# Optimization experiments

Measured on AMD Instinct MI355X. Metric: run time of the kernel, lower is better.

## Reference

```python
import jax, jax.numpy as jnp
import numpy as np

ALPHA1 = 0.1
ALPHA2 = 0.1
NOISE = 0.02
B, T, H, O = 128, 512, 512, 3


def setup_inputs() -> dict:
    key = jax.random.key(0)
    ks = jax.random.split(key, 10)
    return {
        "x": jax.random.normal(ks[0], (B, T, 5), dtype=jnp.float32),
        "wi_stim": jax.random.normal(ks[1], (3, H), dtype=jnp.float32) / np.sqrt(3),
        "wrec11": jax.random.normal(ks[2], (H, H), dtype=jnp.float32) / np.sqrt(H),
        "wi_ctx": jax.random.normal(ks[3], (2, H), dtype=jnp.float32) / np.sqrt(2),
        "wrec22": jax.random.normal(ks[4], (H, H), dtype=jnp.float32) / np.sqrt(H),
        "wrec12": jax.random.normal(ks[5], (H, H), dtype=jnp.float32) / np.sqrt(H),
        "wrec21": jax.random.normal(ks[6], (H, H), dtype=jnp.float32) / np.sqrt(H),
        "wo": jax.random.normal(ks[7], (H, O), dtype=jnp.float32) / np.sqrt(H),
        "noise1": jax.random.normal(ks[8], (T, B, H), dtype=jnp.float32),
        "noise2": jax.random.normal(ks[9], (T, B, H), dtype=jnp.float32),
    }


def reference(x, wi_stim, wrec11, wi_ctx, wrec22, wrec12, wrec21, wo, noise1, noise2):
    # x: [B, T, 5]; noise: [T, B, H] (pre-sampled standard normals, scaled by NOISE)
    xs = jnp.transpose(x[:, :, :3], (1, 0, 2))  # [T, B, 3]
    xc = jnp.transpose(x[:, :, 3:], (1, 0, 2))  # [T, B, 2]

    def step(carry, inp):
        h1, h2 = carry
        xsi, xci, n1, n2 = inp
        h1 = (1 - ALPHA1) * h1 + ALPHA1 * (
            xsi @ wi_stim + jnp.tanh(h1) @ wrec11 + jnp.tanh(h2) @ wrec12 + n1 * NOISE
        )
        # note: h2 update uses the freshly-updated h1 (as in the torch loop)
        h2 = (1 - ALPHA2) * h2 + ALPHA2 * (
            xci @ wi_ctx + jnp.tanh(h1) @ wrec21 + jnp.tanh(h2) @ wrec22 + n2 * NOISE
        )
        return (h1, h2), jnp.tanh(h2) @ wo

    h0 = jnp.zeros((x.shape[0], wrec11.shape[0]), dtype=x.dtype)
    _, out_t = jax.lax.scan(step, (h0, h0), (xs, xc, noise1, noise2))  # [T, B, O]
    return jnp.transpose(out_t, (1, 0, 2))  # [B, T, O]
```

## Files before the change

### kernel.cpp

```cpp
#include <hip/hip_runtime.h>
#include <hip/hip_bf16.h>

#define TT 512
#define BB 128
#define HH 512
#define NGROUP 8
#define NSLICE 8
#define ALPHA 0.1f
#define NOISE_S 0.02f

typedef __attribute__((ext_vector_type(8))) short short8;
typedef __attribute__((ext_vector_type(8))) _Float16 half8;
typedef __attribute__((ext_vector_type(4))) float f32x4;

#define WPACK_CH 132096
#define PUB1_B (WPACK_CH * 16)
#define PUB2_B (PUB1_B + NGROUP * 32768)

__device__ __forceinline__ unsigned short f2h(float f) {
  return __builtin_bit_cast(unsigned short, (_Float16)f);
}

__device__ __forceinline__ float fast_tanh(float x) {
  float e = __builtin_amdgcn_exp2f(x * 2.8853900817779268f);
  return 1.0f - 2.0f * __builtin_amdgcn_rcpf(e + 1.0f);
}

__device__ __forceinline__ f32x4 mfma16(short8 a, short8 b, f32x4 c) {
  return __builtin_amdgcn_mfma_f32_16x16x32_f16(
      __builtin_bit_cast(half8, a), __builtin_bit_cast(half8, b), c, 0, 0, 0);
}

__global__ void pack_weights(const float* __restrict__ w11, const float* __restrict__ w12,
                             const float* __restrict__ w21, const float* __restrict__ w22,
                             const float* __restrict__ wo, unsigned short* __restrict__ dst) {
  int idx = blockIdx.x * 256 + threadIdx.x;
  if (idx < 131072) {
    int which = idx >> 16;
    int c0 = idx & 65535;
    int kt = c0 >> 11, rem = c0 & 2047;
    int nt = rem >> 6, lane = rem & 63;
    const float* wlo = which ? w21 : w11;
    const float* whi = which ? w22 : w12;
    unsigned short* p = dst + (size_t)idx * 8;
    int n = nt * 16 + (lane & 15);
    int kb = kt * 32 + ((lane >> 4) & 3) * 8;
#pragma unroll
    for (int i = 0; i < 8; ++i) {
      int k = kb + i;
      float v = (k < HH) ? wlo[k * HH + n] : whi[(k - HH) * HH + n];
      p[i] = f2h(v);
    }
  } else if (idx < 132096) {
    int c0 = idx - 131072;
    int kt = c0 >> 6, lane = c0 & 63;
    unsigned short* p = dst + (size_t)131072 * 8 + (size_t)c0 * 8;
    int n = lane & 15;
    int kb = kt * 32 + ((lane >> 4) & 3) * 8;
#pragma unroll
    for (int i = 0; i < 8; ++i) {
      float v = (n < 3) ? wo[(kb + i) * 3 + n] : 0.0f;
      p[i] = f2h(v);
    }
  }
}

__global__ void zero_ws(int* __restrict__ p, int n) {
  for (int i = blockIdx.x * 256 + threadIdx.x; i < n; i += gridDim.x * 256)
    p[i] = 0;
}

__global__ __launch_bounds__(256, 1)
void rnn_main(const float* __restrict__ x, const float* __restrict__ wi_stim,
              const float* __restrict__ wi_ctx, const float* __restrict__ noise1,
              const float* __restrict__ noise2, char* __restrict__ ws,
              float* __restrict__ out) {
  __shared__ __align__(16) unsigned short T1buf[16 * 512];
  __shared__ __align__(16) unsigned short T2buf[16 * 512];
  __shared__ __align__(16) unsigned short WOlds[16 * 512];
  __shared__ float xstage[2][16][5];

  const int tid = threadIdx.x;
  const int w = tid >> 6, lane = tid & 63;
  const int c16 = lane & 15, kh = lane >> 4;
  const int g = blockIdx.x & (NGROUP - 1);
  const int slice = blockIdx.x >> 3;
  const int nt = slice * 4 + w;
  const int n0 = nt * 16;
  const int b0 = g * 16;
  const int lrow0 = kh * 4;

  const short8* __restrict__ WC = (const short8*)ws;
  unsigned* __restrict__ pub1 = (unsigned*)(ws + PUB1_B) + g * 8192;
  unsigned* __restrict__ pub2 = (unsigned*)(ws + PUB2_B) + g * 8192;

  short8 z = {0, 0, 0, 0, 0, 0, 0, 0};
  for (int i = tid; i < 1024; i += 256) {
    ((short8*)T1buf)[i] = z;
    ((short8*)T2buf)[i] = z;
  }
#pragma unroll
  for (int c = 0; c < 4; ++c) {
    int kt = w * 4 + c;
    short8 v = WC[131072 + kt * 64 + lane];
    *(short8*)&WOlds[kt * 512 + lane * 8] = v;
  }
  if (tid < 80) {
    int b = tid / 5, c = tid % 5;
    xstage[0][b][c] = x[((size_t)(b0 + b) * TT + 0) * 5 + c];
  }

  short8 wA[32], wB[32];
#pragma unroll
  for (int kt = 0; kt < 32; ++kt) {
    wA[kt] = WC[kt * 2048 + nt * 64 + lane];
    wB[kt] = WC[65536 + kt * 2048 + nt * 64 + lane];
  }
#pragma unroll
  for (int kt = 0; kt < 32; ++kt) {
    asm volatile("" : "+v"(wA[kt]));
    asm volatile("" : "+v"(wB[kt]));
  }

  float wis[3], wic[2];
#pragma unroll
  for (int c = 0; c < 3; ++c) wis[c] = wi_stim[c * HH + n0 + c16];
#pragma unroll
  for (int c = 0; c < 2; ++c) wic[c] = wi_ctx[c * HH + n0 + c16];

  float h1[4] = {0, 0, 0, 0}, h2[4] = {0, 0, 0, 0};

  const int kt_p = nt >> 1;
  const int hi = (((nt & 1) * 16) + c16) >> 3;
  const int ci = c16 & 7;

  auto stage_poll = [&](const unsigned* pubw, unsigned short* Tbuf, unsigned exp) {
    unsigned long long v[4][4];
    bool ok;
    do {
      ok = true;
#pragma unroll
      for (int c = 0; c < 4; ++c) {
        const unsigned long long* src =
            (const unsigned long long*)(pubw + ((w * 4 + c) << 9)) + lane * 4;
#pragma unroll
        for (int j = 0; j < 4; ++j) {
          v[c][j] = __hip_atomic_load(&src[j], __ATOMIC_RELAXED,
                                      __HIP_MEMORY_SCOPE_AGENT);
          ok &= (((unsigned)(v[c][j] >> 16) & 0xffffu) >= exp);
          ok &= ((unsigned)(v[c][j] >> 48) >= exp);
        }
      }
    } while (!ok);
    __builtin_amdgcn_sched_barrier(0);
    asm volatile("" ::: "memory");
#pragma unroll
    for (int c = 0; c < 4; ++c) {
      unsigned long long u0 = (v[c][0] & 0xffffull)
                            | (((v[c][0] >> 32) & 0xffffull) << 16)
                            | ((v[c][1] & 0xffffull) << 32)
                            | (((v[c][1] >> 32) & 0xffffull) << 48);
      unsigned long long u1 = (v[c][2] & 0xffffull)
                            | (((v[c][2] >> 32) & 0xffffull) << 16)
                            | ((v[c][3] & 0xffffull) << 32)
                            | (((v[c][3] >> 32) & 0xffffull) << 48);
      *(unsigned long long*)&Tbuf[(w * 4 + c) * 512 + lane * 8] = u0;
      *(unsigned long long*)&Tbuf[(w * 4 + c) * 512 + lane * 8 + 4] = u1;
    }
  };

  __syncthreads();

  for (int t = 0; t < TT; ++t) {
    const int buf = t & 1;
    const unsigned tagA = (unsigned)(t + 1) << 16;

    float n1v[4];
#pragma unroll
    for (int r = 0; r < 4; ++r)
      n1v[r] = noise1[((size_t)t * BB + b0 + lrow0 + r) * HH + n0 + c16];

    f32x4 aA = {0, 0, 0, 0}, aB = {0, 0, 0, 0};
#pragma unroll
    for (int kt = 0; kt < 16; ++kt) {
      short8 a1 = *(const short8*)&T1buf[kt * 512 + lane * 8];
      aA = mfma16(a1, wA[kt], aA);
    }
    stage_poll(pub2, T2buf, (unsigned)t);
    __syncthreads();
#pragma unroll
    for (int kt = 0; kt < 16; ++kt) {
      short8 a2 = *(const short8*)&T2buf[kt * 512 + lane * 8];
      aB = mfma16(a2, wA[16 + kt], aB);
    }

    if (t > 0 && slice == ((t - 1) & 7) && w == 0) {
      f32x4 ao = {0, 0, 0, 0};
#pragma unroll
      for (int kt = 0; kt < 16; ++kt) {
        short8 a2 = *(const short8*)&T2buf[kt * 512 + lane * 8];
        short8 bo = *(const short8*)&WOlds[kt * 512 + lane * 8];
        ao = mfma16(a2, bo, ao);
      }
      if (c16 < 3) {
#pragma unroll
        for (int r = 0; r < 4; ++r)
          out[((size_t)(b0 + lrow0 + r) * TT + (t - 1)) * 3 + c16] = ao[r];
      }
    }

    unsigned short tp[4];
#pragma unroll
    for (int r = 0; r < 4; ++r) {
      float pre = aA[r] + aB[r]
                + wis[0] * xstage[buf][lrow0 + r][0]
                + wis[1] * xstage[buf][lrow0 + r][1]
                + wis[2] * xstage[buf][lrow0 + r][2]
                + NOISE_S * n1v[r];
      float h = (1.0f - ALPHA) * h1[r] + ALPHA * pre;
      h1[r] = h;
      tp[r] = f2h(fast_tanh(h));
    }
#pragma unroll
    for (int r = 0; r < 4; ++r)
      __hip_atomic_store(&pub1[kt_p * 512 + (lrow0 + r + hi * 16) * 8 + ci],
                         tagA | tp[r], __ATOMIC_RELAXED, __HIP_MEMORY_SCOPE_AGENT);

    float n2v[4];
#pragma unroll
    for (int r = 0; r < 4; ++r)
      n2v[r] = noise2[((size_t)t * BB + b0 + lrow0 + r) * HH + n0 + c16];

    f32x4 bA = {0, 0, 0, 0}, bB = {0, 0, 0, 0};
#pragma unroll
    for (int kt = 0; kt < 16; ++kt) {
      short8 a2 = *(const short8*)&T2buf[kt * 512 + lane * 8];
      bB = mfma16(a2, wB[16 + kt], bB);
    }
    stage_poll(pub1, T1buf, (unsigned)(t + 1));
    if (t + 1 < TT && tid < 80) {
      int b = tid / 5, c = tid % 5;
      xstage[buf ^ 1][b][c] = x[((size_t)(b0 + b) * TT + (t + 1)) * 5 + c];
    }
    __syncthreads();
#pragma unroll
    for (int kt = 0; kt < 16; ++kt) {
      short8 a1 = *(const short8*)&T1buf[kt * 512 + lane * 8];
      bA = mfma16(a1, wB[kt], bA);
    }
#pragma unroll
    for (int r = 0; r < 4; ++r) {
      float pre = bA[r] + bB[r]
                + wic[0] * xstage[buf][lrow0 + r][3]
                + wic[1] * xstage[buf][lrow0 + r][4]
                + NOISE_S * n2v[r];
      float h = (1.0f - ALPHA) * h2[r] + ALPHA * pre;
      h2[r] = h;
      tp[r] = f2h(fast_tanh(h));
    }
#pragma unroll
    for (int r = 0; r < 4; ++r)
      __hip_atomic_store(&pub2[kt_p * 512 + (lrow0 + r + hi * 16) * 8 + ci],
                         tagA | tp[r], __ATOMIC_RELAXED, __HIP_MEMORY_SCOPE_AGENT);
  }

  if (slice == ((TT - 1) & 7)) {
    stage_poll(pub2, T2buf, (unsigned)TT);
    __syncthreads();
    if (w == 0) {
      f32x4 ao = {0, 0, 0, 0};
#pragma unroll
      for (int kt = 0; kt < 16; ++kt) {
        short8 a2 = *(const short8*)&T2buf[kt * 512 + lane * 8];
        short8 bo = *(const short8*)&WOlds[kt * 512 + lane * 8];
        ao = mfma16(a2, bo, ao);
      }
      if (c16 < 3) {
#pragma unroll
        for (int r = 0; r < 4; ++r)
          out[((size_t)(b0 + lrow0 + r) * TT + (TT - 1)) * 3 + c16] = ao[r];
      }
    }
  }
}

extern "C" void kernel_launch(void* const* d_in, const int* in_sizes, int n_in,
                              void* d_out, int out_size, void* d_ws, size_t ws_size,
                              hipStream_t stream) {
  const float* x       = (const float*)d_in[0];
  const float* wi_stim = (const float*)d_in[1];
  const float* w11     = (const float*)d_in[2];
  const float* wi_ctx  = (const float*)d_in[3];
  const float* w22     = (const float*)d_in[4];
  const float* w12     = (const float*)d_in[5];
  const float* w21     = (const float*)d_in[6];
  const float* wo      = (const float*)d_in[7];
  const float* n1      = (const float*)d_in[8];
  const float* n2      = (const float*)d_in[9];
  char* ws = (char*)d_ws;

  int nz = (NGROUP * 32768 * 2) / 4;
  zero_ws<<<64, 256, 0, stream>>>((int*)(ws + PUB1_B), nz);
  pack_weights<<<516, 256, 0, stream>>>(w11, w12, w21, w22, wo,
                                        (unsigned short*)ws);
  rnn_main<<<NSLICE * NGROUP, 256, 0, stream>>>(x, wi_stim, wi_ctx, n1, n2, ws,
                                                (float*)d_out);
}
```

Before: 3.578 ms.

## Process two batch groups per block to interleave independent recurrences

Each block now handles two independent 16-row batch groups instead of one, which halves the grid to 32 blocks. Per step, the block alternates between the two groups' h1 and h2 phases, so one group's cross-block poll latency can be hidden behind the other group's MFMA work. The cost is twice the serial MFMA and tanh work per block, more syncthreads per step, and fewer CUs in use.

```diff
diff --git a/kernel.cpp b/kernel.cpp
--- a/kernel.cpp
+++ b/kernel.cpp
@@ -6,6 +6,7 @@
 #define HH 512
 #define NGROUP 8
 #define NSLICE 8
+#define GPB 2
 #define ALPHA 0.1f
 #define NOISE_S 0.02f
 
@@ -75,27 +76,29 @@
               const float* __restrict__ wi_ctx, const float* __restrict__ noise1,
               const float* __restrict__ noise2, char* __restrict__ ws,
               float* __restrict__ out) {
-  __shared__ __align__(16) unsigned short T1buf[16 * 512];
-  __shared__ __align__(16) unsigned short T2buf[16 * 512];
+  __shared__ __align__(16) unsigned short T1buf[2][16 * 512];
+  __shared__ __align__(16) unsigned short T2buf[2][16 * 512];
   __shared__ __align__(16) unsigned short WOlds[16 * 512];
-  __shared__ float xstage[2][16][5];
+  __shared__ float xstage[2][2][16][5];
 
   const int tid = threadIdx.x;
   const int w = tid >> 6, lane = tid & 63;
   const int c16 = lane & 15, kh = lane >> 4;
-  const int g = blockIdx.x & (NGROUP - 1);
-  const int slice = blockIdx.x >> 3;
+  const int slice = blockIdx.x >> 2;
+  const int gp = blockIdx.x & 3;
   const int nt = slice * 4 + w;
   const int n0 = nt * 16;
-  const int b0 = g * 16;
   const int lrow0 = kh * 4;
 
   const short8* __restrict__ WC = (const short8*)ws;
-  unsigned* __restrict__ pub1 = (unsigned*)(ws + PUB1_B) + g * 8192;
-  unsigned* __restrict__ pub2 = (unsigned*)(ws + PUB2_B) + g * 8192;
+  unsigned* const pub1g[2] = {(unsigned*)(ws + PUB1_B) + gp * 8192,
+                              (unsigned*)(ws + PUB1_B) + (gp + 4) * 8192};
+  unsigned* const pub2g[2] = {(unsigned*)(ws + PUB2_B) + gp * 8192,
+                              (unsigned*)(ws + PUB2_B) + (gp + 4) * 8192};
+  const int b0g[2] = {gp * 16, (gp + 4) * 16};
 
   short8 z = {0, 0, 0, 0, 0, 0, 0, 0};
-  for (int i = tid; i < 1024; i += 256) {
+  for (int i = tid; i < 2048; i += 256) {
     ((short8*)T1buf)[i] = z;
     ((short8*)T2buf)[i] = z;
   }
@@ -105,9 +108,10 @@
     short8 v = WC[131072 + kt * 64 + lane];
     *(short8*)&WOlds[kt * 512 + lane * 8] = v;
   }
-  if (tid < 80) {
-    int b = tid / 5, c = tid % 5;
-    xstage[0][b][c] = x[((size_t)(b0 + b) * TT + 0) * 5 + c];
+  if (tid < 160) {
+    int gi = tid / 80, rem = tid % 80;
+    int b = rem / 5, c = rem % 5;
+    xstage[0][gi][b][c] = x[((size_t)(b0g[gi] + b) * TT + 0) * 5 + c];
   }
 
   short8 wA[32], wB[32];
@@ -128,11 +132,13 @@
 #pragma unroll
   for (int c = 0; c < 2; ++c) wic[c] = wi_ctx[c * HH + n0 + c16];
 
-  float h1[4] = {0, 0, 0, 0}, h2[4] = {0, 0, 0, 0};
+  float h1[2][4] = {{0, 0, 0, 0}, {0, 0, 0, 0}};
+  float h2[2][4] = {{0, 0, 0, 0}, {0, 0, 0, 0}};
 
   const int kt_p = nt >> 1;
   const int hi = (((nt & 1) * 16) + c16) >> 3;
   const int ci = c16 & 7;
+  const int pslot = kt_p * 512 + (lrow0 + hi * 16) * 8 + ci;
 
   auto stage_poll = [&](const unsigned* pubw, unsigned short* Tbuf, unsigned exp) {
     unsigned long long v[4][4];
@@ -173,112 +179,125 @@
 
   for (int t = 0; t < TT; ++t) {
     const int buf = t & 1;
-    const unsigned tagA = (unsigned)(t + 1) << 16;
-
-    float n1v[4];
-#pragma unroll
-    for (int r = 0; r < 4; ++r)
-      n1v[r] = noise1[((size_t)t * BB + b0 + lrow0 + r) * HH + n0 + c16];
-
-    f32x4 aA = {0, 0, 0, 0}, aB = {0, 0, 0, 0};
-#pragma unroll
-    for (int kt = 0; kt < 16; ++kt) {
-      short8 a1 = *(const short8*)&T1buf[kt * 512 + lane * 8];
-      aA = mfma16(a1, wA[kt], aA);
-    }
-    stage_poll(pub2, T2buf, (unsigned)t);
+    const unsigned tagN = (unsigned)(t + 1) << 16;
+
+#pragma unroll
+    for (int gi = 0; gi < 2; ++gi) {
+      float n1v[4];
+#pragma unroll
+      for (int r = 0; r < 4; ++r)
+        n1v[r] = noise1[((size_t)t * BB + b0g[gi] + lrow0 + r) * HH + n0 + c16];
+
+      f32x4 aA = {0, 0, 0, 0}, aB = {0, 0, 0, 0};
+#pragma unroll
+      for (int kt = 0; kt < 16; ++kt) {
+        short8 a1 = *(const short8*)&T1buf[gi][kt * 512 + lane * 8];
+        aA = mfma16(a1, wA[kt], aA);
+      }
+      stage_poll(pub2g[gi], T2buf[gi], (unsigned)t);
+      __syncthreads();
+#pragma unroll
+      for (int kt = 0; kt < 16; ++kt) {
+        short8 a2 = *(const short8*)&T2buf[gi][kt * 512 + lane * 8];
+        aB = mfma16(a2, wA[16 + kt], aB);
+      }
+
+      if (t > 0 && slice == ((t - 1) & 7) && w == gi) {
+        f32x4 ao = {0, 0, 0, 0};
+#pragma unroll
+        for (int kt = 0; kt < 16; ++kt) {
+          short8 a2 = *(const short8*)&T2buf[gi][kt * 512 + lane * 8];
+          short8 bo = *(const short8*)&WOlds[kt * 512 + lane * 8];
+          ao = mfma16(a2, bo, ao);
+        }
+        if (c16 < 3) {
+#pragma unroll
+          for (int r = 0; r < 4; ++r)
+            out[((size_t)(b0g[gi] + lrow0 + r) * TT + (t - 1)) * 3 + c16] = ao[r];
+        }
+      }
+
+      unsigned short tp[4];
+#pragma unroll
+      for (int r = 0; r < 4; ++r) {
+        float pre = aA[r] + aB[r]
+                  + wis[0] * xstage[buf][gi][lrow0 + r][0]
+                  + wis[1] * xstage[buf][gi][lrow0 + r][1]
+                  + wis[2] * xstage[buf][gi][lrow0 + r][2]
+                  + NOISE_S * n1v[r];
+        float h = (1.0f - ALPHA) * h1[gi][r] + ALPHA * pre;
+        h1[gi][r] = h;
+        tp[r] = f2h(fast_tanh(h));
+      }
+#pragma unroll
+      for (int r = 0; r < 4; ++r)
+        __hip_atomic_store(&pub1g[gi][pslot + r * 8], tagN | tp[r],
+                           __ATOMIC_RELAXED, __HIP_MEMORY_SCOPE_AGENT);
+    }
+
+#pragma unroll
+    for (int gi = 0; gi < 2; ++gi) {
+      float n2v[4];
+#pragma unroll
+      for (int r = 0; r < 4; ++r)
+        n2v[r] = noise2[((size_t)t * BB + b0g[gi] + lrow0 + r) * HH + n0 + c16];
+
+      f32x4 bA = {0, 0, 0, 0}, bB = {0, 0, 0, 0};
+#pragma unroll
+      for (int kt = 0; kt < 16; ++kt) {
+        short8 a2 = *(const short8*)&T2buf[gi][kt * 512 + lane * 8];
+        bB = mfma16(a2, wB[16 + kt], bB);
+      }
+      stage_poll(pub1g[gi], T1buf[gi], (unsigned)(t + 1));
+      if (gi == 1 && t + 1 < TT && tid < 160) {
+        int gj = tid / 80, rem = tid % 80;
+        int b = rem / 5, c = rem % 5;
+        xstage[buf ^ 1][gj][b][c] = x[((size_t)(b0g[gj] + b) * TT + (t + 1)) * 5 + c];
+      }
+      __syncthreads();
+#pragma unroll
+      for (int kt = 0; kt < 16; ++kt) {
+        short8 a1 = *(const short8*)&T1buf[gi][kt * 512 + lane * 8];
+        bA = mfma16(a1, wB[kt], bA);
+      }
+      unsigned short tp[4];
+#pragma unroll
+      for (int r = 0; r < 4; ++r) {
+        float pre = bA[r] + bB[r]
+                  + wic[0] * xstage[buf][gi][lrow0 + r][3]
+                  + wic[1] * xstage[buf][gi][lrow0 + r][4]
+                  + NOISE_S * n2v[r];
+        float h = (1.0f - ALPHA) * h2[gi][r] + ALPHA * pre;
+        h2[gi][r] = h;
+        tp[r] = f2h(fast_tanh(h));
+      }
+#pragma unroll
+      for (int r = 0; r < 4; ++r)
+        __hip_atomic_store(&pub2g[gi][pslot + r * 8], tagN | tp[r],
+                           __ATOMIC_RELAXED, __HIP_MEMORY_SCOPE_AGENT);
+    }
+  }
+
+  if (slice == ((TT - 1) & 7)) {
+#pragma unroll
+    for (int gi = 0; gi < 2; ++gi)
+      stage_poll(pub2g[gi], T2buf[gi], (unsigned)TT);
     __syncthreads();
 #pragma unroll
-    for (int kt = 0; kt < 16; ++kt) {
-      short8 a2 = *(const short8*)&T2buf[kt * 512 + lane * 8];
-      aB = mfma16(a2, wA[16 + kt], aB);
-    }
-
-    if (t > 0 && slice == ((t - 1) & 7) && w == 0) {
-      f32x4 ao = {0, 0, 0, 0};
-#pragma unroll
-      for (int kt = 0; kt < 16; ++kt) {
-        short8 a2 = *(const short8*)&T2buf[kt * 512 + lane * 8];
-        short8 bo = *(const short8*)&WOlds[kt * 512 + lane * 8];
-        ao = mfma16(a2, bo, ao);
-      }
-      if (c16 < 3) {
-#pragma unroll
-        for (int r = 0; r < 4; ++r)
-          out[((size_t)(b0 + lrow0 + r) * TT + (t - 1)) * 3 + c16] = ao[r];
-      }
-    }
-
-    unsigned short tp[4];
-#pragma unroll
-    for (int r = 0; r < 4; ++r) {
-      float pre = aA[r] + aB[r]
-                + wis[0] * xstage[buf][lrow0 + r][0]
-                + wis[1] * xstage[buf][lrow0 + r][1]
-                + wis[2] * xstage[buf][lrow0 + r][2]
-                + NOISE_S * n1v[r];
-      float h = (1.0f - ALPHA) * h1[r] + ALPHA * pre;
-      h1[r] = h;
-      tp[r] = f2h(fast_tanh(h));
-    }
-#pragma unroll
-    for (int r = 0; r < 4; ++r)
-      __hip_atomic_store(&pub1[kt_p * 512 + (lrow0 + r + hi * 16) * 8 + ci],
-                         tagA | tp[r], __ATOMIC_RELAXED, __HIP_MEMORY_SCOPE_AGENT);
-
-    float n2v[4];
-#pragma unroll
-    for (int r = 0; r < 4; ++r)
-      n2v[r] = noise2[((size_t)t * BB + b0 + lrow0 + r) * HH + n0 + c16];
-
-    f32x4 bA = {0, 0, 0, 0}, bB = {0, 0, 0, 0};
-#pragma unroll
-    for (int kt = 0; kt < 16; ++kt) {
-      short8 a2 = *(const short8*)&T2buf[kt * 512 + lane * 8];
-      bB = mfma16(a2, wB[16 + kt], bB);
-    }
-    stage_poll(pub1, T1buf, (unsigned)(t + 1));
-    if (t + 1 < TT && tid < 80) {
-      int b = tid / 5, c = tid % 5;
-      xstage[buf ^ 1][b][c] = x[((size_t)(b0 + b) * TT + (t + 1)) * 5 + c];
-    }
-    __syncthreads();
-#pragma unroll
-    for (int kt = 0; kt < 16; ++kt) {
-      short8 a1 = *(const short8*)&T1buf[kt * 512 + lane * 8];
-      bA = mfma16(a1, wB[kt], bA);
-    }
-#pragma unroll
-    for (int r = 0; r < 4; ++r) {
-      float pre = bA[r] + bB[r]
-                + wic[0] * xstage[buf][lrow0 + r][3]
-                + wic[1] * xstage[buf][lrow0 + r][4]
-                + NOISE_S * n2v[r];
-      float h = (1.0f - ALPHA) * h2[r] + ALPHA * pre;
-      h2[r] = h;
-      tp[r] = f2h(fast_tanh(h));
-    }
-#pragma unroll
-    for (int r = 0; r < 4; ++r)
-      __hip_atomic_store(&pub2[kt_p * 512 + (lrow0 + r + hi * 16) * 8 + ci],
-                         tagA | tp[r], __ATOMIC_RELAXED, __HIP_MEMORY_SCOPE_AGENT);
-  }
-
-  if (slice == ((TT - 1) & 7)) {
-    stage_poll(pub2, T2buf, (unsigned)TT);
-    __syncthreads();
-    if (w == 0) {
-      f32x4 ao = {0, 0, 0, 0};
-#pragma unroll
-      for (int kt = 0; kt < 16; ++kt) {
-        short8 a2 = *(const short8*)&T2buf[kt * 512 + lane * 8];
-        short8 bo = *(const short8*)&WOlds[kt * 512 + lane * 8];
-        ao = mfma16(a2, bo, ao);
-      }
-      if (c16 < 3) {
-#pragma unroll
-        for (int r = 0; r < 4; ++r)
-          out[((size_t)(b0 + lrow0 + r) * TT + (TT - 1)) * 3 + c16] = ao[r];
+    for (int gi = 0; gi < 2; ++gi) {
+      if (w == gi) {
+        f32x4 ao = {0, 0, 0, 0};
+#pragma unroll
+        for (int kt = 0; kt < 16; ++kt) {
+          short8 a2 = *(const short8*)&T2buf[gi][kt * 512 + lane * 8];
+          short8 bo = *(const short8*)&WOlds[kt * 512 + lane * 8];
+          ao = mfma16(a2, bo, ao);
+        }
+        if (c16 < 3) {
+#pragma unroll
+          for (int r = 0; r < 4; ++r)
+            out[((size_t)(b0g[gi] + lrow0 + r) * TT + (TT - 1)) * 3 + c16] = ao[r];
+        }
       }
     }
   }
@@ -303,6 +322,6 @@
   zero_ws<<<64, 256, 0, stream>>>((int*)(ws + PUB1_B), nz);
   pack_weights<<<516, 256, 0, stream>>>(w11, w12, w21, w22, wo,
                                         (unsigned short*)ws);
-  rnn_main<<<NSLICE * NGROUP, 256, 0, stream>>>(x, wi_stim, wi_ctx, n1, n2, ws,
-                                                (float*)d_out);
-}
+  rnn_main<<<NSLICE * (NGROUP / GPB), 256, 0, stream>>>(x, wi_stim, wi_ctx,
+                                                        n1, n2, ws, (float*)d_out);
+}
```

Result: slower. 5.464 ms (+52.7%).

## Poll published hidden state directly into per-wave register fragments, dropping LDS staging

Applied to the files above, without the earlier changes.

Each wave now polls all 16 k-tiles of the published tanh(h) buffer itself and packs them straight into MFMA A-fragments in registers. This removes the shared-memory staging buffers and the block-wide __syncthreads between the poll and the matmul. The recurrent weights are no longer pinned in VGPRs; they are re-read from global memory (L2) every step. x values and noise2 are also loaded per thread each step instead of through LDS. The trade-off is 4x more atomic polling traffic per block and heavy weight reloads per step, in exchange for removing block barriers and freeing registers.

```diff
diff --git a/kernel.cpp b/kernel.cpp
--- a/kernel.cpp
+++ b/kernel.cpp
@@ -12,6 +12,7 @@
 typedef __attribute__((ext_vector_type(8))) short short8;
 typedef __attribute__((ext_vector_type(8))) _Float16 half8;
 typedef __attribute__((ext_vector_type(4))) float f32x4;
+typedef __attribute__((ext_vector_type(4))) unsigned u32x4;
 
 #define WPACK_CH 132096
 #define PUB1_B (WPACK_CH * 16)
@@ -75,10 +76,7 @@
               const float* __restrict__ wi_ctx, const float* __restrict__ noise1,
               const float* __restrict__ noise2, char* __restrict__ ws,
               float* __restrict__ out) {
-  __shared__ __align__(16) unsigned short T1buf[16 * 512];
-  __shared__ __align__(16) unsigned short T2buf[16 * 512];
   __shared__ __align__(16) unsigned short WOlds[16 * 512];
-  __shared__ float xstage[2][16][5];
 
   const int tid = threadIdx.x;
   const int w = tid >> 6, lane = tid & 63;
@@ -94,33 +92,12 @@
   unsigned* __restrict__ pub1 = (unsigned*)(ws + PUB1_B) + g * 8192;
   unsigned* __restrict__ pub2 = (unsigned*)(ws + PUB2_B) + g * 8192;
 
-  short8 z = {0, 0, 0, 0, 0, 0, 0, 0};
-  for (int i = tid; i < 1024; i += 256) {
-    ((short8*)T1buf)[i] = z;
-    ((short8*)T2buf)[i] = z;
-  }
 #pragma unroll
   for (int c = 0; c < 4; ++c) {
     int kt = w * 4 + c;
     short8 v = WC[131072 + kt * 64 + lane];
     *(short8*)&WOlds[kt * 512 + lane * 8] = v;
   }
-  if (tid < 80) {
-    int b = tid / 5, c = tid % 5;
-    xstage[0][b][c] = x[((size_t)(b0 + b) * TT + 0) * 5 + c];
-  }
-
-  short8 wA[32], wB[32];
-#pragma unroll
-  for (int kt = 0; kt < 32; ++kt) {
-    wA[kt] = WC[kt * 2048 + nt * 64 + lane];
-    wB[kt] = WC[65536 + kt * 2048 + nt * 64 + lane];
-  }
-#pragma unroll
-  for (int kt = 0; kt < 32; ++kt) {
-    asm volatile("" : "+v"(wA[kt]));
-    asm volatile("" : "+v"(wB[kt]));
-  }
 
   float wis[3], wic[2];
 #pragma unroll
@@ -129,78 +106,87 @@
   for (int c = 0; c < 2; ++c) wic[c] = wi_ctx[c * HH + n0 + c16];
 
   float h1[4] = {0, 0, 0, 0}, h2[4] = {0, 0, 0, 0};
+
+  short8 t1f[16], t2f[16];
+  short8 z = {0, 0, 0, 0, 0, 0, 0, 0};
+#pragma unroll
+  for (int kt = 0; kt < 16; ++kt) { t1f[kt] = z; t2f[kt] = z; }
 
   const int kt_p = nt >> 1;
   const int hi = (((nt & 1) * 16) + c16) >> 3;
   const int ci = c16 & 7;
-
-  auto stage_poll = [&](const unsigned* pubw, unsigned short* Tbuf, unsigned exp) {
-    unsigned long long v[4][4];
+  const int pslot = kt_p * 512 + (lrow0 + hi * 16) * 8 + ci;
+
+  const short8* __restrict__ WAp = WC + nt * 64 + lane;
+  const short8* __restrict__ WBp = WC + 65536 + nt * 64 + lane;
+
+  auto poll_frags = [&](const unsigned* pubw, short8* frag, unsigned exp) {
+    unsigned rw[16][8];
     bool ok;
     do {
       ok = true;
 #pragma unroll
-      for (int c = 0; c < 4; ++c) {
+      for (int kt = 0; kt < 16; ++kt) {
         const unsigned long long* src =
-            (const unsigned long long*)(pubw + ((w * 4 + c) << 9)) + lane * 4;
+            (const unsigned long long*)(pubw + kt * 512) + lane * 4;
 #pragma unroll
         for (int j = 0; j < 4; ++j) {
-          v[c][j] = __hip_atomic_load(&src[j], __ATOMIC_RELAXED,
-                                      __HIP_MEMORY_SCOPE_AGENT);
-          ok &= (((unsigned)(v[c][j] >> 16) & 0xffffu) >= exp);
-          ok &= ((unsigned)(v[c][j] >> 48) >= exp);
+          unsigned long long v = __hip_atomic_load(&src[j], __ATOMIC_RELAXED,
+                                                   __HIP_MEMORY_SCOPE_AGENT);
+          rw[kt][2 * j]     = (unsigned)v;
+          rw[kt][2 * j + 1] = (unsigned)(v >> 32);
         }
       }
+#pragma unroll
+      for (int kt = 0; kt < 16; ++kt)
+#pragma unroll
+        for (int j = 0; j < 8; ++j) ok &= ((rw[kt][j] >> 16) >= exp);
+      if (!__all(ok)) { __builtin_amdgcn_s_sleep(1); ok = false; }
     } while (!ok);
-    __builtin_amdgcn_sched_barrier(0);
-    asm volatile("" ::: "memory");
-#pragma unroll
-    for (int c = 0; c < 4; ++c) {
-      unsigned long long u0 = (v[c][0] & 0xffffull)
-                            | (((v[c][0] >> 32) & 0xffffull) << 16)
-                            | ((v[c][1] & 0xffffull) << 32)
-                            | (((v[c][1] >> 32) & 0xffffull) << 48);
-      unsigned long long u1 = (v[c][2] & 0xffffull)
-                            | (((v[c][2] >> 32) & 0xffffull) << 16)
-                            | ((v[c][3] & 0xffffull) << 32)
-                            | (((v[c][3] >> 32) & 0xffffull) << 48);
-      *(unsigned long long*)&Tbuf[(w * 4 + c) * 512 + lane * 8] = u0;
-      *(unsigned long long*)&Tbuf[(w * 4 + c) * 512 + lane * 8 + 4] = u1;
+#pragma unroll
+    for (int kt = 0; kt < 16; ++kt) {
+      u32x4 p;
+#pragma unroll
+      for (int q = 0; q < 4; ++q)
+        p[q] = (rw[kt][2 * q + 1] << 16) | (rw[kt][2 * q] & 0xffffu);
+      frag[kt] = __builtin_bit_cast(short8, p);
     }
   };
 
   __syncthreads();
 
   for (int t = 0; t < TT; ++t) {
-    const int buf = t & 1;
-    const unsigned tagA = (unsigned)(t + 1) << 16;
-
-    float n1v[4];
+    const unsigned tagN = (unsigned)(t + 1) << 16;
+
+    float xv[4][5];
 #pragma unroll
     for (int r = 0; r < 4; ++r)
-      n1v[r] = noise1[((size_t)t * BB + b0 + lrow0 + r) * HH + n0 + c16];
+#pragma unroll
+      for (int c = 0; c < 5; ++c)
+        xv[r][c] = x[((size_t)(b0 + lrow0 + r) * TT + t) * 5 + c];
+    float n1v[4], n2v[4];
+#pragma unroll
+    for (int r = 0; r < 4; ++r) {
+      size_t rowoff = ((size_t)t * BB + b0 + lrow0 + r) * HH + n0 + c16;
+      n1v[r] = noise1[rowoff];
+      n2v[r] = noise2[rowoff];
+    }
 
     f32x4 aA = {0, 0, 0, 0}, aB = {0, 0, 0, 0};
 #pragma unroll
-    for (int kt = 0; kt < 16; ++kt) {
-      short8 a1 = *(const short8*)&T1buf[kt * 512 + lane * 8];
-      aA = mfma16(a1, wA[kt], aA);
-    }
-    stage_poll(pub2, T2buf, (unsigned)t);
-    __syncthreads();
-#pragma unroll
-    for (int kt = 0; kt < 16; ++kt) {
-      short8 a2 = *(const short8*)&T2buf[kt * 512 + lane * 8];
-      aB = mfma16(a2, wA[16 + kt], aB);
-    }
+    for (int kt = 0; kt < 16; ++kt)
+      aA = mfma16(t1f[kt], WAp[kt * 2048], aA);
+    poll_frags(pub2, t2f, (unsigned)t);
+#pragma unroll
+    for (int kt = 0; kt < 16; ++kt)
+      aB = mfma16(t2f[kt], WAp[(16 + kt) * 2048], aB);
 
     if (t > 0 && slice == ((t - 1) & 7) && w == 0) {
       f32x4 ao = {0, 0, 0, 0};
 #pragma unroll
       for (int kt = 0; kt < 16; ++kt) {
-        short8 a2 = *(const short8*)&T2buf[kt * 512 + lane * 8];
         short8 bo = *(const short8*)&WOlds[kt * 512 + lane * 8];
-        ao = mfma16(a2, bo, ao);
+        ao = mfma16(t2f[kt], bo, ao);
       }
       if (c16 < 3) {
 #pragma unroll
@@ -213,9 +199,7 @@
 #pragma unroll
     for (int r = 0; r < 4; ++r) {
       float pre = aA[r] + aB[r]
-                + wis[0] * xstage[buf][lrow0 + r][0]
-                + wis[1] * xstage[buf][lrow0 + r][1]
-                + wis[2] * xstage[buf][lrow0 + r][2]
+                + wis[0] * xv[r][0] + wis[1] * xv[r][1] + wis[2] * xv[r][2]
                 + NOISE_S * n1v[r];
       float h = (1.0f - ALPHA) * h1[r] + ALPHA * pre;
       h1[r] = h;
@@ -223,36 +207,21 @@
     }
 #pragma unroll
     for (int r = 0; r < 4; ++r)
-      __hip_atomic_store(&pub1[kt_p * 512 + (lrow0 + r + hi * 16) * 8 + ci],
-                         tagA | tp[r], __ATOMIC_RELAXED, __HIP_MEMORY_SCOPE_AGENT);
-
-    float n2v[4];
-#pragma unroll
-    for (int r = 0; r < 4; ++r)
-      n2v[r] = noise2[((size_t)t * BB + b0 + lrow0 + r) * HH + n0 + c16];
+      __hip_atomic_store(&pub1[pslot + r * 8], tagN | tp[r],
+                         __ATOMIC_RELAXED, __HIP_MEMORY_SCOPE_AGENT);
 
     f32x4 bA = {0, 0, 0, 0}, bB = {0, 0, 0, 0};
 #pragma unroll
-    for (int kt = 0; kt < 16; ++kt) {
-      short8 a2 = *(const short8*)&T2buf[kt * 512 + lane * 8];
-      bB = mfma16(a2, wB[16 + kt], bB);
-    }
-    stage_poll(pub1, T1buf, (unsigned)(t + 1));
-    if (t + 1 < TT && tid < 80) {
-      int b = tid / 5, c = tid % 5;
-      xstage[buf ^ 1][b][c] = x[((size_t)(b0 + b) * TT + (t + 1)) * 5 + c];
-    }
-    __syncthreads();
-#pragma unroll
-    for (int kt = 0; kt < 16; ++kt) {
-      short8 a1 = *(const short8*)&T1buf[kt * 512 + lane * 8];
-      bA = mfma16(a1, wB[kt], bA);
-    }
+    for (int kt = 0; kt < 16; ++kt)
+      bB = mfma16(t2f[kt], WBp[(16 + kt) * 2048], bB);
+    poll_frags(pub1, t1f, (unsigned)(t + 1));
+#pragma unroll
+    for (int kt = 0; kt < 16; ++kt)
+      bA = mfma16(t1f[kt], WBp[kt * 2048], bA);
 #pragma unroll
     for (int r = 0; r < 4; ++r) {
       float pre = bA[r] + bB[r]
-                + wic[0] * xstage[buf][lrow0 + r][3]
-                + wic[1] * xstage[buf][lrow0 + r][4]
+                + wic[0] * xv[r][3] + wic[1] * xv[r][4]
                 + NOISE_S * n2v[r];
       float h = (1.0f - ALPHA) * h2[r] + ALPHA * pre;
       h2[r] = h;
@@ -260,26 +229,22 @@
     }
 #pragma unroll
     for (int r = 0; r < 4; ++r)
-      __hip_atomic_store(&pub2[kt_p * 512 + (lrow0 + r + hi * 16) * 8 + ci],
-                         tagA | tp[r], __ATOMIC_RELAXED, __HIP_MEMORY_SCOPE_AGENT);
-  }
-
-  if (slice == ((TT - 1) & 7)) {
-    stage_poll(pub2, T2buf, (unsigned)TT);
-    __syncthreads();
-    if (w == 0) {
-      f32x4 ao = {0, 0, 0, 0};
-#pragma unroll
-      for (int kt = 0; kt < 16; ++kt) {
-        short8 a2 = *(const short8*)&T2buf[kt * 512 + lane * 8];
-        short8 bo = *(const short8*)&WOlds[kt * 512 + lane * 8];
-        ao = mfma16(a2, bo, ao);
-      }
-      if (c16 < 3) {
-#pragma unroll
-        for (int r = 0; r < 4; ++r)
-          out[((size_t)(b0 + lrow0 + r) * TT + (TT - 1)) * 3 + c16] = ao[r];
-      }
+      __hip_atomic_store(&pub2[pslot + r * 8], tagN | tp[r],
+                         __ATOMIC_RELAXED, __HIP_MEMORY_SCOPE_AGENT);
+  }
+
+  if (slice == ((TT - 1) & 7) && w == 0) {
+    poll_frags(pub2, t2f, (unsigned)TT);
+    f32x4 ao = {0, 0, 0, 0};
+#pragma unroll
+    for (int kt = 0; kt < 16; ++kt) {
+      short8 bo = *(const short8*)&WOlds[kt * 512 + lane * 8];
+      ao = mfma16(t2f[kt], bo, ao);
+    }
+    if (c16 < 3) {
+#pragma unroll
+      for (int r = 0; r < 4; ++r)
+        out[((size_t)(b0 + lrow0 + r) * TT + (TT - 1)) * 3 + c16] = ao[r];
     }
   }
 }
```

Measured after the change: 10.70 ms. +199.1%, slower.

## Stream recurrent weights from global and issue flag polls early to overlap latency

Applied to the files above, without the earlier changes.

Drops the 64 register-resident short8 weight fragments per lane and reads the recurrent weights from global memory (via cache) inside each MFMA loop. It also splits the cross-block poll into an early issue, placed right after publishing and before the independent MFMA half, and a later check, so the poll load latency overlaps compute. Both noise loads are hoisted to the start of the step. The aim is lower register pressure and hidden polling latency. The cost is a global/L2 weight fetch on every timestep, which may lengthen the serial critical path of this latency-bound recurrence.

```diff
diff --git a/kernel.cpp b/kernel.cpp
--- a/kernel.cpp
+++ b/kernel.cpp
@@ -110,18 +110,6 @@
     xstage[0][b][c] = x[((size_t)(b0 + b) * TT + 0) * 5 + c];
   }
 
-  short8 wA[32], wB[32];
-#pragma unroll
-  for (int kt = 0; kt < 32; ++kt) {
-    wA[kt] = WC[kt * 2048 + nt * 64 + lane];
-    wB[kt] = WC[65536 + kt * 2048 + nt * 64 + lane];
-  }
-#pragma unroll
-  for (int kt = 0; kt < 32; ++kt) {
-    asm volatile("" : "+v"(wA[kt]));
-    asm volatile("" : "+v"(wB[kt]));
-  }
-
   float wis[3], wic[2];
 #pragma unroll
   for (int c = 0; c < 3; ++c) wis[c] = wi_stim[c * HH + n0 + c16];
@@ -133,65 +121,84 @@
   const int kt_p = nt >> 1;
   const int hi = (((nt & 1) * 16) + c16) >> 3;
   const int ci = c16 & 7;
-
-  auto stage_poll = [&](const unsigned* pubw, unsigned short* Tbuf, unsigned exp) {
-    unsigned long long v[4][4];
-    bool ok;
-    do {
-      ok = true;
-#pragma unroll
-      for (int c = 0; c < 4; ++c) {
-        const unsigned long long* src =
-            (const unsigned long long*)(pubw + ((w * 4 + c) << 9)) + lane * 4;
+  const int pslot = kt_p * 512 + (lrow0 + hi * 16) * 8 + ci;
+
+  const short8* __restrict__ WAp = WC + nt * 64 + lane;
+  const short8* __restrict__ WBp = WC + 65536 + nt * 64 + lane;
+
+  unsigned long long pv1[4][4], pv2[4][4];
+
+  auto issue_poll = [&](const unsigned* pubw, unsigned long long (*pv)[4]) {
+#pragma unroll
+    for (int c = 0; c < 4; ++c) {
+      const unsigned long long* src =
+          (const unsigned long long*)(pubw + ((w * 4 + c) << 9)) + lane * 4;
+#pragma unroll
+      for (int j = 0; j < 4; ++j)
+        pv[c][j] = __hip_atomic_load(&src[j], __ATOMIC_RELAXED,
+                                     __HIP_MEMORY_SCOPE_AGENT);
+    }
+  };
+
+  auto finish_poll = [&](const unsigned* pubw, unsigned long long (*pv)[4],
+                         unsigned short* Tbuf, unsigned exp) {
+    for (;;) {
+      bool ok = true;
+#pragma unroll
+      for (int c = 0; c < 4; ++c)
 #pragma unroll
         for (int j = 0; j < 4; ++j) {
-          v[c][j] = __hip_atomic_load(&src[j], __ATOMIC_RELAXED,
-                                      __HIP_MEMORY_SCOPE_AGENT);
-          ok &= (((unsigned)(v[c][j] >> 16) & 0xffffu) >= exp);
-          ok &= ((unsigned)(v[c][j] >> 48) >= exp);
+          ok &= (((unsigned)(pv[c][j] >> 16) & 0xffffu) >= exp);
+          ok &= ((unsigned)(pv[c][j] >> 48) >= exp);
         }
-      }
-    } while (!ok);
+      if (ok) break;
+      issue_poll(pubw, pv);
+    }
     __builtin_amdgcn_sched_barrier(0);
     asm volatile("" ::: "memory");
 #pragma unroll
     for (int c = 0; c < 4; ++c) {
-      unsigned long long u0 = (v[c][0] & 0xffffull)
-                            | (((v[c][0] >> 32) & 0xffffull) << 16)
-                            | ((v[c][1] & 0xffffull) << 32)
-                            | (((v[c][1] >> 32) & 0xffffull) << 48);
-      unsigned long long u1 = (v[c][2] & 0xffffull)
-                            | (((v[c][2] >> 32) & 0xffffull) << 16)
-                            | ((v[c][3] & 0xffffull) << 32)
-                            | (((v[c][3] >> 32) & 0xffffull) << 48);
+      unsigned long long u0 = (pv[c][0] & 0xffffull)
+                            | (((pv[c][0] >> 32) & 0xffffull) << 16)
+                            | ((pv[c][1] & 0xffffull) << 32)
+                            | (((pv[c][1] >> 32) & 0xffffull) << 48);
+      unsigned long long u1 = (pv[c][2] & 0xffffull)
+                            | (((pv[c][2] >> 32) & 0xffffull) << 16)
+                            | ((pv[c][3] & 0xffffull) << 32)
+                            | (((pv[c][3] >> 32) & 0xffffull) << 48);
       *(unsigned long long*)&Tbuf[(w * 4 + c) * 512 + lane * 8] = u0;
       *(unsigned long long*)&Tbuf[(w * 4 + c) * 512 + lane * 8 + 4] = u1;
     }
   };
 
   __syncthreads();
+  issue_poll(pub2, pv2);
+  __builtin_amdgcn_sched_barrier(0);
 
   for (int t = 0; t < TT; ++t) {
     const int buf = t & 1;
-    const unsigned tagA = (unsigned)(t + 1) << 16;
-
-    float n1v[4];
-#pragma unroll
-    for (int r = 0; r < 4; ++r)
-      n1v[r] = noise1[((size_t)t * BB + b0 + lrow0 + r) * HH + n0 + c16];
+    const unsigned tagN = (unsigned)(t + 1) << 16;
+
+    float n1v[4], n2v[4];
+#pragma unroll
+    for (int r = 0; r < 4; ++r) {
+      size_t rowoff = ((size_t)t * BB + b0 + lrow0 + r) * HH + n0 + c16;
+      n1v[r] = noise1[rowoff];
+      n2v[r] = noise2[rowoff];
+    }
 
     f32x4 aA = {0, 0, 0, 0}, aB = {0, 0, 0, 0};
 #pragma unroll
     for (int kt = 0; kt < 16; ++kt) {
       short8 a1 = *(const short8*)&T1buf[kt * 512 + lane * 8];
-      aA = mfma16(a1, wA[kt], aA);
-    }
-    stage_poll(pub2, T2buf, (unsigned)t);
+      aA = mfma16(a1, WAp[kt * 2048], aA);
+    }
+    finish_poll(pub2, pv2, T2buf, (unsigned)t);
     __syncthreads();
 #pragma unroll
     for (int kt = 0; kt < 16; ++kt) {
       short8 a2 = *(const short8*)&T2buf[kt * 512 + lane * 8];
-      aB = mfma16(a2, wA[16 + kt], aB);
+      aB = mfma16(a2, WAp[(16 + kt) * 2048], aB);
     }
 
     if (t > 0 && slice == ((t - 1) & 7) && w == 0) {
@@ -223,21 +230,18 @@
     }
 #pragma unroll
     for (int r = 0; r < 4; ++r)
-      __hip_atomic_store(&pub1[kt_p * 512 + (lrow0 + r + hi * 16) * 8 + ci],
-                         tagA | tp[r], __ATOMIC_RELAXED, __HIP_MEMORY_SCOPE_AGENT);
-
-    float n2v[4];
-#pragma unroll
-    for (int r = 0; r < 4; ++r)
-      n2v[r] = noise2[((size_t)t * BB + b0 + lrow0 + r) * HH + n0 + c16];
+      __hip_atomic_store(&pub1[pslot + r * 8], tagN | tp[r],
+                         __ATOMIC_RELAXED, __HIP_MEMORY_SCOPE_AGENT);
+    issue_poll(pub1, pv1);
+    __builtin_amdgcn_sched_barrier(0);
 
     f32x4 bA = {0, 0, 0, 0}, bB = {0, 0, 0, 0};
 #pragma unroll
     for (int kt = 0; kt < 16; ++kt) {
       short8 a2 = *(const short8*)&T2buf[kt * 512 + lane * 8];
-      bB = mfma16(a2, wB[16 + kt], bB);
-    }
-    stage_poll(pub1, T1buf, (unsigned)(t + 1));
+      bB = mfma16(a2, WBp[(16 + kt) * 2048], bB);
+    }
+    finish_poll(pub1, pv1, T1buf, (unsigned)(t + 1));
     if (t + 1 < TT && tid < 80) {
       int b = tid / 5, c = tid % 5;
       xstage[buf ^ 1][b][c] = x[((size_t)(b0 + b) * TT + (t + 1)) * 5 + c];
@@ -246,7 +250,7 @@
 #pragma unroll
     for (int kt = 0; kt < 16; ++kt) {
       short8 a1 = *(const short8*)&T1buf[kt * 512 + lane * 8];
-      bA = mfma16(a1, wB[kt], bA);
+      bA = mfma16(a1, WBp[kt * 2048], bA);
     }
 #pragma unroll
     for (int r = 0; r < 4; ++r) {
@@ -260,12 +264,14 @@
     }
 #pragma unroll
     for (int r = 0; r < 4; ++r)
-      __hip_atomic_store(&pub2[kt_p * 512 + (lrow0 + r + hi * 16) * 8 + ci],
-                         tagA | tp[r], __ATOMIC_RELAXED, __HIP_MEMORY_SCOPE_AGENT);
+      __hip_atomic_store(&pub2[pslot + r * 8], tagN | tp[r],
+                         __ATOMIC_RELAXED, __HIP_MEMORY_SCOPE_AGENT);
+    issue_poll(pub2, pv2);
+    __builtin_amdgcn_sched_barrier(0);
   }
 
   if (slice == ((TT - 1) & 7)) {
-    stage_poll(pub2, T2buf, (unsigned)TT);
+    finish_poll(pub2, pv2, T2buf, (unsigned)TT);
     __syncthreads();
     if (w == 0) {
       f32x4 ao = {0, 0, 0, 0};
```

After: 6.869 ms. +92.0%, slower.
